# Performance work log

Hardware: AMD Instinct MI355X
Metric: run time of the kernel (lower is better)

## Reference

```python
import jax, jax.numpy as jnp
import numpy as np

B, T, S, H = 4, 2048, 2048, 1024


def setup_inputs() -> dict:
    key = jax.random.key(0)
    k1, k2, k3, k4, k5, k6 = jax.random.split(key, 6)
    scale_w = 1.0 / np.sqrt(H)  # roughly nn.Linear init scale
    return {
        "tar": jax.random.normal(k1, (B, T, H), jnp.float32),
        "src": jax.random.normal(k2, (B, S, H), jnp.float32),
        "ori_src": jax.random.normal(k3, (B, S, H), jnp.float32),
        "Wq": jax.random.normal(k4, (H, H), jnp.float32) * scale_w,
        "Wk": jax.random.normal(k5, (H, H), jnp.float32) * scale_w,
        "Wv": jax.random.normal(k6, (H, H), jnp.float32) * scale_w,
    }


def reference(tar, src, ori_src, Wq, Wk, Wv):
    # nn.Linear(bias=False): y = x @ W.T
    q = src @ Wq.T        # (B, S, H)
    k = tar @ Wk.T        # (B, T, H)
    v = ori_src @ Wv.T    # (B, S, H)
    scaling = jnp.asarray(H ** 0.5, q.dtype)
    # scores[b,t,s] = q[b,s] . k[b,t] / sqrt(H); torch softmax was over dim=-2 (the S axis)
    scores = jnp.einsum('bsh,bth->bts', q, k) / scaling  # (B, T, S)
    attn = jax.nn.softmax(scores, axis=-1)               # softmax over src positions s
    context = jnp.einsum('bts,bsh->bth', attn, v)        # (B, T, H)
    return context, attn
```

## Files before the change

### kernel.cpp

```cpp
#include <hip/hip_runtime.h>

#define BB 4
#define TT 2048
#define SS 2048
#define HH 1024

typedef unsigned short u16;
typedef __attribute__((ext_vector_type(4))) unsigned short u16x4;
typedef __attribute__((ext_vector_type(8))) short bf16x8;
typedef __attribute__((ext_vector_type(4))) float f32x4;

#define TILE_U16 (128 * 32)

__device__ __forceinline__ u16 f2bf(float f) {
    union { float f; unsigned u; } a; a.f = f;
    unsigned r = a.u + 0x7fffu + ((a.u >> 16) & 1u);
    return (u16)(r >> 16);
}
__device__ __forceinline__ float bf2f(u16 h) {
    union { unsigned u; float f; } a; a.u = ((unsigned)h) << 16;
    return a.f;
}


__device__ __forceinline__ void stage_bf16(const u16* gbase, int ld, int row0, int k0,
                                           u16* lds, int tid) {
#pragma unroll
    for (int c = 0; c < 2; ++c) {
        int g = c * 256 + tid;
        int row = g >> 2, col = g & 3;
        const u16* gp = gbase + (size_t)(row0 + row) * ld + k0 + col * 8;
        u16* lp = lds + (size_t)(c * 256 + (tid & ~63)) * 8;
        __builtin_amdgcn_global_load_lds((__attribute__((address_space(1))) const void*)gp,
                                         (__attribute__((address_space(3))) void*)lp,
                                         16, 0, 0);
    }
}

__device__ __forceinline__ void stage_f32(const float* gbase, int ld, int row0, int k0,
                                          u16* lds, int tid) {
#pragma unroll
    for (int c = 0; c < 4; ++c) {
        int f = c * 256 + tid;
        int row = f >> 3, c4 = f & 7;
        const float4 v = *(const float4*)(gbase + (size_t)(row0 + row) * ld + k0 + c4 * 4);
        u16x4 o;
        o.x = f2bf(v.x); o.y = f2bf(v.y); o.z = f2bf(v.z); o.w = f2bf(v.w);
        *(u16x4*)(lds + row * 32 + c4 * 4) = o;
    }
}

__device__ __forceinline__ void mfma_step(const u16* As, const u16* Bs,
                                          f32x4 acc[4][4], int tid) {
    int lane = tid & 63, quad = lane >> 4, l16 = lane & 15;
    int wm = (tid >> 6) & 1, wn = tid >> 7;
    const u16* Ab = As + (wm * 64 + l16) * 32 + quad * 8;
    const u16* Bb = Bs + (wn * 64 + l16) * 32 + quad * 8;
    bf16x8 af[4], bfr[4];
#pragma unroll
    for (int i = 0; i < 4; ++i) af[i] = *(const bf16x8*)(Ab + i * 512);
#pragma unroll
    for (int j = 0; j < 4; ++j) bfr[j] = *(const bf16x8*)(Bb + j * 512);
#pragma unroll
    for (int i = 0; i < 4; ++i)
#pragma unroll
        for (int j = 0; j < 4; ++j)
            acc[i][j] = __builtin_amdgcn_mfma_f32_16x16x32_bf16(af[i], bfr[j], acc[i][j], 0, 0, 0);
}

__device__ __forceinline__ void zero_acc(f32x4 acc[4][4]) {
#pragma unroll
    for (int i = 0; i < 4; ++i)
#pragma unroll
        for (int j = 0; j < 4; ++j)
            acc[i][j] = (f32x4){0.f, 0.f, 0.f, 0.f};
}

__device__ __forceinline__ void gemm_loop_bf16(const u16* A, int lda, int bm,
                                               const u16* B, int ldb, int bn,
                                               int K, u16* As, u16* Bs,
                                               f32x4 acc[4][4], int tid) {
    stage_bf16(A, lda, bm, 0, As, tid);
    stage_bf16(B, ldb, bn, 0, Bs, tid);
    const int kiters = K / 32;
    for (int kit = 0; kit < kiters; ++kit) {
        const int cur = (kit & 1) * TILE_U16, nxt = TILE_U16 - cur;
        __syncthreads();
        if (kit + 1 < kiters) {
            stage_bf16(A, lda, bm, (kit + 1) * 32, As + nxt, tid);
            stage_bf16(B, ldb, bn, (kit + 1) * 32, Bs + nxt, tid);
        }
        mfma_step(As + cur, Bs + cur, acc, tid);
    }
}

__device__ __forceinline__ void gemm_loop_f32a(const float* A, int lda, int bm,
                                               const u16* B, int ldb, int bn,
                                               int K, u16* As, u16* Bs,
                                               f32x4 acc[4][4], int tid) {
    stage_f32(A, lda, bm, 0, As, tid);
    stage_bf16(B, ldb, bn, 0, Bs, tid);
    const int kiters = K / 32;
    for (int kit = 0; kit < kiters; ++kit) {
        const int cur = (kit & 1) * TILE_U16, nxt = TILE_U16 - cur;
        __syncthreads();
        if (kit + 1 < kiters) {
            stage_f32(A, lda, bm, (kit + 1) * 32, As + nxt, tid);
            stage_bf16(B, ldb, bn, (kit + 1) * 32, Bs + nxt, tid);
        }
        mfma_step(As + cur, Bs + cur, acc, tid);
    }
}


__global__ __launch_bounds__(256) void cvt3_kernel(const float* __restrict__ p0,
                                                   const float* __restrict__ p1,
                                                   const float* __restrict__ p2,
                                                   u16* __restrict__ o0,
                                                   u16* __restrict__ o1,
                                                   u16* __restrict__ o2) {
    const int z = blockIdx.y;
    const float* in = (z == 0) ? p0 : (z == 1) ? p1 : p2;
    u16* out = (z == 0) ? o0 : (z == 1) ? o1 : o2;
    int i = (blockIdx.x * 256 + threadIdx.x) * 4;
    float4 v = *(const float4*)(in + i);
    u16x4 o;
    o.x = f2bf(v.x); o.y = f2bf(v.y); o.z = f2bf(v.z); o.w = f2bf(v.w);
    *(u16x4*)(out + i) = o;
}

__global__ __launch_bounds__(256) void cvt_kernel(const float* __restrict__ in,
                                                  u16* __restrict__ out) {
    int i = (blockIdx.x * 256 + threadIdx.x) * 4;
    float4 v = *(const float4*)(in + i);
    u16x4 o;
    o.x = f2bf(v.x); o.y = f2bf(v.y); o.z = f2bf(v.z); o.w = f2bf(v.w);
    *(u16x4*)(out + i) = o;
}

__global__ __launch_bounds__(256) void zero_kernel(float* __restrict__ p) {
    int i = (blockIdx.x * 256 + threadIdx.x) * 4;
    *(float4*)(p + i) = (float4){0.f, 0.f, 0.f, 0.f};
}


__device__ __forceinline__ void stage_half(const u16* g, int ld, u16* lds, int tid) {
#pragma unroll
    for (int c = 0; c < 2; ++c) {
        int gr = c * 512 + tid;
        int r = gr >> 3, k8 = gr & 7;
        const u16* gp = g + (size_t)r * ld + ((k8 ^ (r & 7)) << 3);
        u16* lp = lds + (size_t)(c * 512 + (tid & ~63)) * 8;
        __builtin_amdgcn_global_load_lds((__attribute__((address_space(1))) const void*)gp,
                                         (__attribute__((address_space(3))) void*)lp,
                                         16, 0, 0);
    }
}

#define G256_RD_A(qm)                                                         \
    _Pragma("unroll") for (int i = 0; i < 4; ++i) {                           \
        const u16* _p = Ab + ((qm) * 64 + i * 16 + l16) * 64;                 \
        a[i][0] = *(const bf16x8*)(_p + co0);                                 \
        a[i][1] = *(const bf16x8*)(_p + co1);                                 \
    }

#define G256_RD_B(qn)                                                         \
    _Pragma("unroll") for (int j = 0; j < J2; ++j) {                          \
        const u16* _p = Bb + (rB0 + (qn) * J2 * 16 + j * 16 + l16) * 64;      \
        b[j][0] = *(const bf16x8*)(_p + co0);                                 \
        b[j][1] = *(const bf16x8*)(_p + co1);                                 \
    }

#define G256_MFMA(qm, qn)                                                     \
    __builtin_amdgcn_s_barrier();                                             \
    asm volatile("s_waitcnt lgkmcnt(0)" ::: "memory");                        \
    __builtin_amdgcn_s_setprio(1);                                            \
    _Pragma("unroll") for (int i = 0; i < 4; ++i)                             \
        _Pragma("unroll") for (int j = 0; j < J2; ++j) {                      \
            acc[(qm) * 4 + i][(qn) * J2 + j] =                                \
                __builtin_amdgcn_mfma_f32_16x16x32_bf16(                      \
                    a[i][0], b[j][0], acc[(qm) * 4 + i][(qn) * J2 + j], 0, 0, 0); \
            acc[(qm) * 4 + i][(qn) * J2 + j] =                                \
                __builtin_amdgcn_mfma_f32_16x16x32_bf16(                      \
                    a[i][1], b[j][1], acc[(qm) * 4 + i][(qn) * J2 + j], 0, 0, 0); \
        }                                                                     \
    __builtin_amdgcn_s_setprio(0);

template <int BN>
__device__ __forceinline__ void g256_loop(const u16* __restrict__ A, int lda,
                                          const u16* __restrict__ B, int ldb, int K,
                                          u16* sm, f32x4 (&acc)[8][BN / 64], int tid) {
    constexpr int J2 = BN / 128;
    constexpr int ATILE = 16384;
    constexpr int BTILE = BN * 64;
    u16* As = sm;
    u16* Bs = sm + 2 * ATILE;
    const int lane = tid & 63, wid = tid >> 6;
    const int wm = wid >> 2, wn = wid & 3;
    const int l16 = lane & 15, quad = lane >> 4;
    const int co0 = (quad ^ (l16 & 7)) * 8;
    const int co1 = ((4 | quad) ^ (l16 & 7)) * 8;
    const int rB0 = (BN == 256) ? (wn & 1) * 64 : wn * 32;
    const int NT = K >> 6;

#pragma unroll
    for (int i = 0; i < 8; ++i)
#pragma unroll
        for (int j = 0; j < BN / 64; ++j) acc[i][j] = (f32x4){0.f, 0.f, 0.f, 0.f};

    stage_half(A, lda, As, tid);
    stage_half(A + (size_t)128 * lda, lda, As + 8192, tid);
    stage_half(B, ldb, Bs, tid);
    if (BN == 256) stage_half(B + (size_t)128 * ldb, ldb, Bs + 8192, tid);
    stage_half(A + 64, lda, As + ATILE, tid);
    stage_half(A + (size_t)128 * lda + 64, lda, As + ATILE + 8192, tid);
    asm volatile("s_waitcnt vmcnt(4)" ::: "memory");
    __builtin_amdgcn_s_barrier();
    __builtin_amdgcn_sched_barrier(0);

    const u16* Aw = As + wm * 8192;
    const u16* Bw = Bs + ((BN == 256) ? (wn >> 1) * 8192 : 0);

    for (int t = 0; t < NT; ++t) {
        const u16* Ab = Aw + (t & 1) * ATILE;
        const u16* Bb = Bw + (t & 1) * BTILE;
        const int nx = (t + 1) & 1;
        bf16x8 a[4][2], b[J2][2];
        G256_RD_A(0)
        G256_RD_B(0)
        if (t + 1 < NT) stage_half(B + (size_t)(t + 1) * 64, ldb, Bs + nx * BTILE, tid);
        G256_MFMA(0, 0)
        __builtin_amdgcn_s_barrier();
        G256_RD_B(1)
        if (BN == 256 && t + 1 < NT)
            stage_half(B + (size_t)128 * ldb + (size_t)(t + 1) * 64, ldb,
                       Bs + nx * BTILE + 8192, tid);
        G256_MFMA(0, 1)
        __builtin_amdgcn_s_barrier();
        G256_RD_A(1)
        G256_MFMA(1, 1)
        __builtin_amdgcn_s_barrier();
        G256_RD_B(0)
        if (t + 2 < NT) {
            stage_half(A + (size_t)(t + 2) * 64, lda, As + (t & 1) * ATILE, tid);
            stage_half(A + (size_t)128 * lda + (size_t)(t + 2) * 64, lda,
                       As + (t & 1) * ATILE + 8192, tid);
        }
        G256_MFMA(1, 0)
        if (t + 2 < NT) asm volatile("s_waitcnt vmcnt(4)" ::: "memory");
        else            asm volatile("s_waitcnt vmcnt(0)" ::: "memory");
        __builtin_amdgcn_s_barrier();
        __builtin_amdgcn_sched_barrier(0);
    }
}

__global__ __launch_bounds__(512, 2) void proj256_kernel(
        const u16* __restrict__ A0, const u16* __restrict__ A1, const u16* __restrict__ A2,
        const u16* __restrict__ W0, const u16* __restrict__ W1, const u16* __restrict__ W2,
        u16* __restrict__ qb, u16* __restrict__ kb, u16* __restrict__ vT) {
    __shared__ u16 sm[2 * 16384 + 2 * 128 * 64];
    const int bid = blockIdx.x;
    const int wg = (bid & 7) * 96 + (bid >> 3);
    const int z = wg >> 8, rr = wg & 255;
    const int by = rr >> 3, bx = rr & 7;
    const u16* A = ((z == 0) ? A0 : (z == 1) ? A1 : A2) + (size_t)(by * 256) * HH;
    const u16* W = ((z == 0) ? W0 : (z == 1) ? W1 : W2) + (size_t)(bx * 128) * HH;
    const int tid = threadIdx.x;
    f32x4 acc[8][2];
    g256_loop<128>(A, HH, W, HH, HH, sm, acc, tid);

    const int lane = tid & 63, quad = lane >> 4, l16 = lane & 15, wid = tid >> 6;
    const int wm = wid >> 2, wn = wid & 3;
    const int m0 = by * 256 + wm * 128, n0 = bx * 128 + wn * 32;
    if (z < 2) {
        u16* C = z ? kb : qb;
#pragma unroll
        for (int i = 0; i < 8; ++i)
#pragma unroll
            for (int j = 0; j < 2; ++j) {
                const int m = m0 + i * 16 + quad * 4;
                const int n = n0 + j * 16 + l16;
#pragma unroll
                for (int r = 0; r < 4; ++r)
                    C[(size_t)(m + r) * HH + n] = f2bf(acc[i][j][r]);
            }
    } else {
#pragma unroll
        for (int i = 0; i < 8; ++i)
#pragma unroll
            for (int j = 0; j < 2; ++j) {
                const int m = m0 + i * 16 + quad * 4;
                const int n = n0 + j * 16 + l16;
                u16x4 o;
                o.x = f2bf(acc[i][j][0]); o.y = f2bf(acc[i][j][1]);
                o.z = f2bf(acc[i][j][2]); o.w = f2bf(acc[i][j][3]);
                *(u16x4*)(vT + (size_t)n * (BB * SS) + m) = o;
            }
    }
}

__global__ __launch_bounds__(512, 2) void scores256_kernel(
        const u16* __restrict__ qb, const u16* __restrict__ kb,
        u16* __restrict__ eb, float* __restrict__ rowsum) {
    __shared__ u16 sm[2 * 16384 + 2 * 256 * 64];
    const int bid = blockIdx.x;
    const int wg = (bid & 7) * 32 + (bid >> 3);
    const int b = wg >> 6, by = (wg >> 3) & 7, bx = wg & 7;
    const u16* A = kb + (size_t)b * TT * HH + (size_t)(by * 256) * HH;
    const u16* Q = qb + (size_t)b * SS * HH + (size_t)(bx * 256) * HH;
    const int tid = threadIdx.x;
    f32x4 acc[8][4];
    g256_loop<256>(A, HH, Q, HH, HH, sm, acc, tid);

    const int lane = tid & 63, quad = lane >> 4, l16 = lane & 15, wid = tid >> 6;
    const int wm = wid >> 2, wn = wid & 3;
    const int m0 = by * 256 + wm * 128, n0 = bx * 256 + wn * 64;
#pragma unroll
    for (int i = 0; i < 8; ++i)
#pragma unroll
        for (int j = 0; j < 4; ++j)
#pragma unroll
            for (int r = 0; r < 4; ++r)
                acc[i][j][r] = __expf(acc[i][j][r] * 0.03125f);
    u16* E = eb + (size_t)b * TT * SS;
#pragma unroll
    for (int i = 0; i < 8; ++i)
#pragma unroll
        for (int j = 0; j < 4; ++j) {
            const int m = m0 + i * 16 + quad * 4;
            const int n = n0 + j * 16 + l16;
#pragma unroll
            for (int r = 0; r < 4; ++r)
                E[(size_t)(m + r) * SS + n] = f2bf(acc[i][j][r]);
        }
    const size_t Rb = (size_t)b * TT + m0 + quad * 4;
#pragma unroll
    for (int i = 0; i < 8; ++i)
#pragma unroll
        for (int r = 0; r < 4; ++r) {
            float s = acc[i][0][r] + acc[i][1][r] + acc[i][2][r] + acc[i][3][r];
            s += __shfl_xor(s, 1, 64);
            s += __shfl_xor(s, 2, 64);
            s += __shfl_xor(s, 4, 64);
            s += __shfl_xor(s, 8, 64);
            if (l16 == 0) atomicAdd(&rowsum[Rb + i * 16 + r], s);
        }
}

__global__ __launch_bounds__(512, 2) void ctx256_kernel(
        const u16* __restrict__ eb, const u16* __restrict__ vT,
        const float* __restrict__ rowsum, float* __restrict__ out) {
    __shared__ u16 sm[2 * 16384 + 2 * 128 * 64];
    const int bid = blockIdx.x;
    const int wg = (bid & 7) * 32 + (bid >> 3);
    const int b = wg >> 6, by = (wg >> 3) & 7, bx = wg & 7;
    const u16* A = eb + (size_t)b * TT * SS + (size_t)(by * 256) * SS;
    const u16* V = vT + (size_t)b * SS + (size_t)(bx * 128) * (size_t)(BB * SS);
    const int tid = threadIdx.x;
    f32x4 acc[8][2];
    g256_loop<128>(A, SS, V, BB * SS, SS, sm, acc, tid);

    const int lane = tid & 63, quad = lane >> 4, l16 = lane & 15, wid = tid >> 6;
    const int wm = wid >> 2, wn = wid & 3;
    const int m0 = by * 256 + wm * 128, n0 = bx * 128 + wn * 32;
    float* C = out + (size_t)b * TT * HH;
    const float* RS = rowsum + (size_t)b * TT;
#pragma unroll
    for (int i = 0; i < 8; ++i)
#pragma unroll
        for (int r = 0; r < 4; ++r) {
            const int m = m0 + i * 16 + quad * 4 + r;
            const float scl = 1.0f / RS[m];
#pragma unroll
            for (int j = 0; j < 2; ++j)
                C[(size_t)m * HH + n0 + j * 16 + l16] = acc[i][j][r] * scl;
        }
}


template <int AF32, int NZ>
__global__ __launch_bounds__(256, 4) void proj_kernel(const float* __restrict__ F0,
                                                      const float* __restrict__ F1,
                                                      const float* __restrict__ F2,
                                                      const u16* __restrict__ A0,
                                                      const u16* __restrict__ A1,
                                                      const u16* __restrict__ A2,
                                                      const u16* __restrict__ W0,
                                                      const u16* __restrict__ W1,
                                                      const u16* __restrict__ W2,
                                                      u16* __restrict__ qb,
                                                      u16* __restrict__ kb,
                                                      u16* __restrict__ vT,
                                                      int zbase) {
    __shared__ u16 As[2 * TILE_U16];
    __shared__ u16 Bs[2 * TILE_U16];
    const int bid = blockIdx.x;
    const int xcd = bid & 7, slot = bid >> 3;
    const int bx = slot & 7;
    const int grp = xcd * (NZ * 8) + (slot >> 3);
    const int z = zbase + (NZ == 3 ? (grp >> 6) : 0);
    const int by = grp & 63;

    const float* AF = (z == 0) ? F0 : (z == 1) ? F1 : F2;
    const u16* AB = (z == 0) ? A0 : (z == 1) ? A1 : A2;
    const u16* W = (z == 0) ? W0 : (z == 1) ? W1 : W2;
    const int bm = by * 128, bn = bx * 128;
    const int tid = threadIdx.x;

    f32x4 acc[4][4];
    zero_acc(acc);
    if (AF32) gemm_loop_f32a(AF, HH, bm, W, HH, bn, HH, As, Bs, acc, tid);
    else      gemm_loop_bf16(AB, HH, bm, W, HH, bn, HH, As, Bs, acc, tid);

    const int lane = tid & 63, quad = lane >> 4, l16 = lane & 15;
    const int wm = (tid >> 6) & 1, wn = tid >> 7;
    const int m0 = bm + wm * 64, n0 = bn + wn * 64;
    if (z < 2) {
        u16* C = (z == 0) ? qb : kb;
#pragma unroll
        for (int i = 0; i < 4; ++i)
#pragma unroll
            for (int j = 0; j < 4; ++j) {
                int m = m0 + i * 16 + quad * 4;
                int n = n0 + j * 16 + l16;
#pragma unroll
                for (int r = 0; r < 4; ++r)
                    C[(size_t)(m + r) * HH + n] = f2bf(acc[i][j][r]);
            }
    } else {
#pragma unroll
        for (int i = 0; i < 4; ++i)
#pragma unroll
            for (int j = 0; j < 4; ++j) {
                int m = m0 + i * 16 + quad * 4;
                int n = n0 + j * 16 + l16;
                u16x4 o;
                o.x = f2bf(acc[i][j][0]); o.y = f2bf(acc[i][j][1]);
                o.z = f2bf(acc[i][j][2]); o.w = f2bf(acc[i][j][3]);
                *(u16x4*)(vT + (size_t)n * (BB * SS) + m) = o;
            }
    }
}

template <int FUSE>
__global__ __launch_bounds__(256, 4) void scores_kernel(const u16* __restrict__ qb,
                                                        const u16* __restrict__ kb,
                                                        float* __restrict__ attn,
                                                        u16* __restrict__ eb,
                                                        float* __restrict__ rowsum) {
    __shared__ u16 As[2 * TILE_U16];
    __shared__ u16 Bs[2 * TILE_U16];
    const int bid = blockIdx.x;
    const int xcd = bid & 7, slot = bid >> 3;
    const int bx = slot & 15;
    const int grp = xcd * 8 + (slot >> 4);
    const int b = grp >> 4, by = grp & 15;

    const u16* A = kb + (size_t)b * TT * HH;
    const u16* Bq = qb + (size_t)b * SS * HH;
    const int bm = by * 128, bn = bx * 128;
    const int tid = threadIdx.x;

    f32x4 acc[4][4];
    zero_acc(acc);
    gemm_loop_bf16(A, HH, bm, Bq, HH, bn, HH, As, Bs, acc, tid);

    const int lane = tid & 63, quad = lane >> 4, l16 = lane & 15;
    const int wm = (tid >> 6) & 1, wn = tid >> 7;
    const int m0 = bm + wm * 64, n0 = bn + wn * 64;

    if (FUSE) {
#pragma unroll
        for (int i = 0; i < 4; ++i)
#pragma unroll
            for (int j = 0; j < 4; ++j)
#pragma unroll
                for (int r = 0; r < 4; ++r)
                    acc[i][j][r] = __expf(acc[i][j][r] * 0.03125f);
        u16* E = eb + (size_t)b * TT * SS;
#pragma unroll
        for (int i = 0; i < 4; ++i)
#pragma unroll
            for (int j = 0; j < 4; ++j) {
                int m = m0 + i * 16 + quad * 4;
                int n = n0 + j * 16 + l16;
#pragma unroll
                for (int r = 0; r < 4; ++r)
                    E[(size_t)(m + r) * SS + n] = f2bf(acc[i][j][r]);
            }
        const size_t Rb = (size_t)b * TT + m0 + quad * 4;
#pragma unroll
        for (int i = 0; i < 4; ++i)
#pragma unroll
            for (int r = 0; r < 4; ++r) {
                float s = acc[i][0][r] + acc[i][1][r] + acc[i][2][r] + acc[i][3][r];
                s += __shfl_xor(s, 1, 64);
                s += __shfl_xor(s, 2, 64);
                s += __shfl_xor(s, 4, 64);
                s += __shfl_xor(s, 8, 64);
                if (l16 == 0) atomicAdd(&rowsum[Rb + i * 16 + r], s);
            }
    } else {
        float* C = attn + (size_t)b * TT * SS;
#pragma unroll
        for (int i = 0; i < 4; ++i)
#pragma unroll
            for (int j = 0; j < 4; ++j) {
                int m = m0 + i * 16 + quad * 4;
                int n = n0 + j * 16 + l16;
#pragma unroll
                for (int r = 0; r < 4; ++r)
                    C[(size_t)(m + r) * SS + n] = acc[i][j][r] * 0.03125f;
            }
    }
}

__global__ __launch_bounds__(256) void norm_kernel(const u16* __restrict__ eb,
                                                   const float* __restrict__ rowsum,
                                                   float* __restrict__ attn) {
    const size_t row = blockIdx.x;
    const float inv = 1.0f / rowsum[row];
    const u16* p = eb + row * SS;
    float* o = attn + row * SS;
    const int tid = threadIdx.x;
#pragma unroll
    for (int c = 0; c < 2; ++c) {
        u16x4 v = *(const u16x4*)(p + c * 1024 + tid * 4);
        float4 f;
        f.x = bf2f(v.x) * inv; f.y = bf2f(v.y) * inv;
        f.z = bf2f(v.z) * inv; f.w = bf2f(v.w) * inv;
        *(float4*)(o + c * 1024 + tid * 4) = f;
    }
}

__global__ __launch_bounds__(256) void softmax_kernel(float* __restrict__ attn,
                                                      u16* __restrict__ attn_bf) {
    const size_t row = blockIdx.x;
    float* p = attn + row * SS;
    const int tid = threadIdx.x;
    float4 a = *(float4*)(p + tid * 4);
    float4 b = *(float4*)(p + 1024 + tid * 4);

    float m = fmaxf(fmaxf(fmaxf(a.x, a.y), fmaxf(a.z, a.w)),
                    fmaxf(fmaxf(b.x, b.y), fmaxf(b.z, b.w)));
#pragma unroll
    for (int off = 32; off > 0; off >>= 1) m = fmaxf(m, __shfl_xor(m, off, 64));
    __shared__ float rmax[4], rsum[4];
    if ((tid & 63) == 0) rmax[tid >> 6] = m;
    __syncthreads();
    m = fmaxf(fmaxf(rmax[0], rmax[1]), fmaxf(rmax[2], rmax[3]));

    a.x = __expf(a.x - m); a.y = __expf(a.y - m);
    a.z = __expf(a.z - m); a.w = __expf(a.w - m);
    b.x = __expf(b.x - m); b.y = __expf(b.y - m);
    b.z = __expf(b.z - m); b.w = __expf(b.w - m);
    float s = a.x + a.y + a.z + a.w + b.x + b.y + b.z + b.w;
#pragma unroll
    for (int off = 32; off > 0; off >>= 1) s += __shfl_xor(s, off, 64);
    if ((tid & 63) == 0) rsum[tid >> 6] = s;
    __syncthreads();
    s = rsum[0] + rsum[1] + rsum[2] + rsum[3];
    float inv = 1.0f / s;

    a.x *= inv; a.y *= inv; a.z *= inv; a.w *= inv;
    b.x *= inv; b.y *= inv; b.z *= inv; b.w *= inv;
    *(float4*)(p + tid * 4) = a;
    *(float4*)(p + 1024 + tid * 4) = b;

    if (attn_bf) {
        u16* pb = attn_bf + row * SS;
        u16x4 oa, ob;
        oa.x = f2bf(a.x); oa.y = f2bf(a.y); oa.z = f2bf(a.z); oa.w = f2bf(a.w);
        ob.x = f2bf(b.x); ob.y = f2bf(b.y); ob.z = f2bf(b.z); ob.w = f2bf(b.w);
        *(u16x4*)(pb + tid * 4) = oa;
        *(u16x4*)(pb + 1024 + tid * 4) = ob;
    }
}

template <int AF32, int SCALE>
__global__ __launch_bounds__(256, 4) void ctx_kernel(const float* __restrict__ attnF,
                                                     const u16* __restrict__ attnB,
                                                     const u16* __restrict__ vT,
                                                     const float* __restrict__ rowsum,
                                                     float* __restrict__ out) {
    __shared__ u16 As[2 * TILE_U16];
    __shared__ u16 Bs[2 * TILE_U16];
    const int bid = blockIdx.x;
    const int xcd = bid & 7, slot = bid >> 3;
    const int bx = slot & 7;
    const int grp = xcd * 8 + (slot >> 3);
    const int b = grp >> 4, by = grp & 15;

    const float* AF = attnF + (size_t)b * TT * SS;
    const u16* AB = attnB + (size_t)b * TT * SS;
    const u16* Bv = vT + (size_t)b * SS;
    float* C = out + (size_t)b * TT * HH;
    const int bm = by * 128, bn = bx * 128;
    const int tid = threadIdx.x;

    f32x4 acc[4][4];
    zero_acc(acc);
    if (AF32) gemm_loop_f32a(AF, SS, bm, Bv, BB * SS, bn, SS, As, Bs, acc, tid);
    else      gemm_loop_bf16(AB, SS, bm, Bv, BB * SS, bn, SS, As, Bs, acc, tid);

    const int lane = tid & 63, quad = lane >> 4, l16 = lane & 15;
    const int wm = (tid >> 6) & 1, wn = tid >> 7;
    const int m0 = bm + wm * 64, n0 = bn + wn * 64;
#pragma unroll
    for (int i = 0; i < 4; ++i)
#pragma unroll
        for (int r = 0; r < 4; ++r) {
            int m = m0 + i * 16 + quad * 4 + r;
            float scl = 1.0f;
            if (SCALE) scl = 1.0f / rowsum[(size_t)b * TT + m];
#pragma unroll
            for (int j = 0; j < 4; ++j) {
                int n = n0 + j * 16 + l16;
                C[(size_t)m * HH + n] = acc[i][j][r] * scl;
            }
        }
}

extern "C" void kernel_launch(void* const* d_in, const int* in_sizes, int n_in,
                              void* d_out, int out_size, void* d_ws, size_t ws_size,
                              hipStream_t stream) {
    const float* tar = (const float*)d_in[0];
    const float* src = (const float*)d_in[1];
    const float* ori = (const float*)d_in[2];
    const float* Wq  = (const float*)d_in[3];
    const float* Wk  = (const float*)d_in[4];
    const float* Wv  = (const float*)d_in[5];

    float* ctx_out  = (float*)d_out;
    float* attn_out = ctx_out + (size_t)BB * TT * HH;

    const size_t M1 = 1024 * 1024;
    u16* ws  = (u16*)d_ws;
    u16* qb  = ws;
    u16* kb  = ws + 8 * M1;
    u16* vT  = ws + 16 * M1;
    u16* wqb = ws + 24 * M1;
    u16* wkb = ws + 25 * M1;
    u16* wvb = ws + 26 * M1;
    u16* inb = ws + 27 * M1;
    u16* eb = inb;
    float* rowsum = (float*)wqb;
    u16* attn_bf = qb;

    const size_t need_fused = (27 + 24) * M1 * 2;
    const size_t need_split = (27 + 8) * M1 * 2;
    const int mode = (ws_size >= need_fused) ? 0 : (ws_size >= need_split) ? 1 : 2;

    cvt3_kernel<<<dim3(1024, 3), 256, 0, stream>>>(Wq, Wk, Wv, wqb, wkb, wvb);

    if (mode == 0) {
        u16* srcb = inb;
        u16* tarb = inb + 8 * M1;
        u16* orib = inb + 16 * M1;
        cvt3_kernel<<<dim3(8192, 3), 256, 0, stream>>>(src, tar, ori, srcb, tarb, orib);
        proj256_kernel<<<768, 512, 0, stream>>>(srcb, tarb, orib, wqb, wkb, wvb, qb, kb, vT);
        zero_kernel<<<8, 256, 0, stream>>>(rowsum);
        scores256_kernel<<<256, 512, 0, stream>>>(qb, kb, eb, rowsum);
        norm_kernel<<<BB * TT, 256, 0, stream>>>(eb, rowsum, attn_out);
        ctx256_kernel<<<256, 512, 0, stream>>>(eb, vT, rowsum, ctx_out);
    } else if (mode == 1) {
        const float* fin[3] = {src, tar, ori};
        for (int z = 0; z < 3; ++z) {
            cvt_kernel<<<8192, 256, 0, stream>>>(fin[z], inb);
            proj_kernel<0, 1><<<512, 256, 0, stream>>>(
                nullptr, nullptr, nullptr, inb, inb, inb, wqb, wkb, wvb, qb, kb, vT, z);
        }
        scores_kernel<0><<<1024, 256, 0, stream>>>(qb, kb, attn_out, nullptr, nullptr);
        softmax_kernel<<<BB * TT, 256, 0, stream>>>(attn_out, attn_bf);
        ctx_kernel<0, 0><<<512, 256, 0, stream>>>(nullptr, attn_bf, vT, nullptr, ctx_out);
    } else {
        proj_kernel<1, 3><<<1536, 256, 0, stream>>>(
            src, tar, ori, nullptr, nullptr, nullptr, wqb, wkb, wvb, qb, kb, vT, 0);
        scores_kernel<0><<<1024, 256, 0, stream>>>(qb, kb, attn_out, nullptr, nullptr);
        softmax_kernel<<<BB * TT, 256, 0, stream>>>(attn_out, nullptr);
        ctx_kernel<1, 0><<<512, 256, 0, stream>>>(attn_out, nullptr, vT, nullptr, ctx_out);
    }
}
```

Measured before the change: 348.5 us.

## Double-buffer LDS fragment registers to overlap reads with MFMA in GEMM loop

Restructures the projection GEMM main loop so A/B fragments are held in two register sets and the next quadrant's LDS reads are issued before the current quadrant's MFMAs. Next-tile fragments are prefetched after the end-of-iteration barrier while the last MFMA block runs. This removes several per-quadrant barriers and lgkmcnt waits, so LDS latency is meant to hide behind matrix math. In exchange it uses more VGPRs, which may pressure occupancy at 512 threads with 2 blocks per CU.

```diff
diff --git a/kernel.cpp b/kernel.cpp
--- a/kernel.cpp
+++ b/kernel.cpp
@@ -157,32 +157,30 @@
     }
 }
 
-#define G256_RD_A(qm)                                                         \
+#define G_RD_A(dst, Abp, qm)                                                  \
     _Pragma("unroll") for (int i = 0; i < 4; ++i) {                           \
-        const u16* _p = Ab + ((qm) * 64 + i * 16 + l16) * 64;                 \
-        a[i][0] = *(const bf16x8*)(_p + co0);                                 \
-        a[i][1] = *(const bf16x8*)(_p + co1);                                 \
-    }
-
-#define G256_RD_B(qn)                                                         \
+        const u16* _p = (Abp) + ((qm) * 64 + i * 16 + l16) * 64;              \
+        dst[i][0] = *(const bf16x8*)(_p + co0);                               \
+        dst[i][1] = *(const bf16x8*)(_p + co1);                               \
+    }
+
+#define G_RD_B(dst, Bbp, qn)                                                  \
     _Pragma("unroll") for (int j = 0; j < J2; ++j) {                          \
-        const u16* _p = Bb + (rB0 + (qn) * J2 * 16 + j * 16 + l16) * 64;      \
-        b[j][0] = *(const bf16x8*)(_p + co0);                                 \
-        b[j][1] = *(const bf16x8*)(_p + co1);                                 \
-    }
-
-#define G256_MFMA(qm, qn)                                                     \
-    __builtin_amdgcn_s_barrier();                                             \
-    asm volatile("s_waitcnt lgkmcnt(0)" ::: "memory");                        \
+        const u16* _p = (Bbp) + (rB0 + (qn) * J2 * 16 + j * 16 + l16) * 64;   \
+        dst[j][0] = *(const bf16x8*)(_p + co0);                               \
+        dst[j][1] = *(const bf16x8*)(_p + co1);                               \
+    }
+
+#define G_MM(af, bf, qm, qn)                                                  \
     __builtin_amdgcn_s_setprio(1);                                            \
     _Pragma("unroll") for (int i = 0; i < 4; ++i)                             \
         _Pragma("unroll") for (int j = 0; j < J2; ++j) {                      \
             acc[(qm) * 4 + i][(qn) * J2 + j] =                                \
                 __builtin_amdgcn_mfma_f32_16x16x32_bf16(                      \
-                    a[i][0], b[j][0], acc[(qm) * 4 + i][(qn) * J2 + j], 0, 0, 0); \
+                    af[i][0], bf[j][0], acc[(qm) * 4 + i][(qn) * J2 + j], 0, 0, 0); \
             acc[(qm) * 4 + i][(qn) * J2 + j] =                                \
                 __builtin_amdgcn_mfma_f32_16x16x32_bf16(                      \
-                    a[i][1], b[j][1], acc[(qm) * 4 + i][(qn) * J2 + j], 0, 0, 0); \
+                    af[i][1], bf[j][1], acc[(qm) * 4 + i][(qn) * J2 + j], 0, 0, 0); \
         }                                                                     \
     __builtin_amdgcn_s_setprio(0);
 
@@ -221,36 +219,50 @@
     const u16* Aw = As + wm * 8192;
     const u16* Bw = Bs + ((BN == 256) ? (wn >> 1) * 8192 : 0);
 
+    bf16x8 a0[4][2], a1[4][2], b0[J2][2], b1[J2][2];
+    {
+        const u16* Ab = Aw;
+        const u16* Bb = Bw;
+        G_RD_A(a0, Ab, 0)
+        G_RD_B(b0, Bb, 0)
+    }
+
     for (int t = 0; t < NT; ++t) {
         const u16* Ab = Aw + (t & 1) * ATILE;
         const u16* Bb = Bw + (t & 1) * BTILE;
         const int nx = (t + 1) & 1;
-        bf16x8 a[4][2], b[J2][2];
-        G256_RD_A(0)
-        G256_RD_B(0)
+        G_RD_A(a1, Ab, 1)
         if (t + 1 < NT) stage_half(B + (size_t)(t + 1) * 64, ldb, Bs + nx * BTILE, tid);
-        G256_MFMA(0, 0)
-        __builtin_amdgcn_s_barrier();
-        G256_RD_B(1)
+        __builtin_amdgcn_sched_barrier(0);
+        G_MM(a0, b0, 0, 0)
+        G_RD_B(b1, Bb, 1)
         if (BN == 256 && t + 1 < NT)
             stage_half(B + (size_t)128 * ldb + (size_t)(t + 1) * 64, ldb,
                        Bs + nx * BTILE + 8192, tid);
-        G256_MFMA(0, 1)
+        __builtin_amdgcn_sched_barrier(0);
+        G_MM(a1, b0, 1, 0)
+        asm volatile("s_waitcnt lgkmcnt(0)" ::: "memory");
+        __builtin_amdgcn_sched_barrier(0);
         __builtin_amdgcn_s_barrier();
-        G256_RD_A(1)
-        G256_MFMA(1, 1)
-        __builtin_amdgcn_s_barrier();
-        G256_RD_B(0)
         if (t + 2 < NT) {
             stage_half(A + (size_t)(t + 2) * 64, lda, As + (t & 1) * ATILE, tid);
             stage_half(A + (size_t)128 * lda + (size_t)(t + 2) * 64, lda,
                        As + (t & 1) * ATILE + 8192, tid);
         }
-        G256_MFMA(1, 0)
+        __builtin_amdgcn_sched_barrier(0);
+        G_MM(a0, b1, 0, 1)
         if (t + 2 < NT) asm volatile("s_waitcnt vmcnt(4)" ::: "memory");
         else            asm volatile("s_waitcnt vmcnt(0)" ::: "memory");
         __builtin_amdgcn_s_barrier();
         __builtin_amdgcn_sched_barrier(0);
+        if (t + 1 < NT) {
+            const u16* An = Aw + nx * ATILE;
+            const u16* Bn = Bw + nx * BTILE;
+            G_RD_A(a0, An, 0)
+            G_RD_B(b0, Bn, 0)
+        }
+        __builtin_amdgcn_sched_barrier(0);
+        G_MM(a1, b1, 1, 1)
     }
 }
 
```

After: 345.1 us. No clear change (-1.0%).
